# Optimization experiments

Measured on AMD Instinct MI355X. Metric: run time of the kernel, lower is better.

The kernel has to match this reference:

```python
import jax, jax.numpy as jnp
import numpy as np

N = 100000   # nodes
E = 3200000  # directed edges (avg degree 32)
T = 2048     # total flattened orders across all moves
M = 256      # number of moves (segments)


def _gat(x, src, dst, Wl, bl, Wr, br, att, b):
    # GATv2Conv (heads=1, eval mode -> attention dropout off), with self loops
    xl = x @ Wl.T + bl              # [N,10]
    xr = x @ Wr.T + br              # [N,10]
    sl = jnp.arange(N)
    s = jnp.concatenate([src, sl])
    d = jnp.concatenate([dst, sl])
    e = jax.nn.leaky_relu(xl[s] + xr[d], 0.2) @ att    # [E+N]
    emax = jax.ops.segment_max(e, d, num_segments=N)
    ex = jnp.exp(e - emax[d])
    den = jax.ops.segment_sum(ex, d, num_segments=N)
    return jax.ops.segment_sum((ex / den[d])[:, None] * xl[s], d, num_segments=N) + b


def setup_inputs() -> dict:
    key = jax.random.key(0)
    ks = iter(jax.random.split(key, 64))
    rn = lambda shape, s=0.1: jax.random.normal(next(ks), shape, jnp.float32) * s
    inp = {}
    inp['x1'] = rn((N, 15), 1.0)
    inp['x2'] = rn((1, 4), 1.0)
    src = jax.random.randint(next(ks), (E,), 0, N, jnp.int32)
    off = jax.random.randint(next(ks), (E,), 1, N, jnp.int32)
    inp['edge_src'] = src
    inp['edge_dst'] = ((src + off) % N).astype(jnp.int32)
    inp['move_type'] = jax.random.randint(next(ks), (T,), 0, 2, jnp.int32)
    inp['m_src'] = jax.random.randint(next(ks), (T,), 0, N, jnp.int32)
    inp['m_dst'] = jax.random.randint(next(ks), (T,), 0, N, jnp.int32)
    inp['m_target'] = jax.random.randint(next(ks), (T,), 0, N, jnp.int32)
    inp['m_armies'] = jax.random.uniform(next(ks), (T,), jnp.float32) * 10.0
    inp['move_id'] = (jnp.arange(T, dtype=jnp.int32) // (T // M))  # sorted, all segments non-empty
    # GATv2 layer params (in dims 15, 25, 25 -> out 10)
    for i, din in [(1, 15), (2, 25), (3, 25)]:
        inp[f'Wl{i}'] = rn((10, din)); inp[f'bl{i}'] = rn((10,))
        inp[f'Wr{i}'] = rn((10, din)); inp[f'br{i}'] = rn((10,))
        inp[f'att{i}'] = rn((10,));   inp[f'bias{i}'] = rn((10,))
    inp['lin_W'] = rn((15, 29)); inp['lin_b'] = rn((15,))
    inp['lin2_W'] = rn((1, 15)); inp['lin2_b'] = rn((1,))
    inp['aaa_W'] = rn((20, 48)); inp['aaa_b'] = rn((20,))
    inp['ccc_W'] = rn((20, 23)); inp['ccc_b'] = rn((20,))
    inp['attl_W'] = rn((1, 20)); inp['attl_b'] = rn((1,))
    inp['pi_W'] = rn((1, 20));   inp['pi_b'] = rn((1,))
    return inp


def reference(x1, x2, edge_src, edge_dst, move_type, m_src, m_dst, m_target, m_armies, move_id,
              Wl1, bl1, Wr1, br1, att1, bias1,
              Wl2, bl2, Wr2, br2, att2, bias2,
              Wl3, bl3, Wr3, br3, att3, bias3,
              lin_W, lin_b, lin2_W, lin2_b, aaa_W, aaa_b, ccc_W, ccc_b,
              attl_W, attl_b, pi_W, pi_b):
    h = jax.nn.relu(_gat(x1, edge_src, edge_dst, Wl1, bl1, Wr1, br1, att1, bias1))
    h = jax.nn.relu(_gat(jnp.concatenate([h, x1], 1), edge_src, edge_dst, Wl2, bl2, Wr2, br2, att2, bias2))
    x = jax.nn.relu(_gat(jnp.concatenate([h, x1], 1), edge_src, edge_dst, Wl3, bl3, Wr3, br3, att3, bias3))

    # per-order features (both branches computed, selected by move_type)
    extra = (0.6 * m_armies - 0.7 * (x1[m_dst, 3] + x1[m_dst, 4]))[:, None]
    feat_a = jnp.concatenate([x[m_src], x[m_dst], x1[m_src, 3:], x1[m_dst, 1:], m_armies[:, None], extra], axis=1)  # [T,48]
    a_out = jax.nn.relu(feat_a @ aaa_W.T + aaa_b)
    feat_d = jnp.concatenate([x[m_target], x1[m_target, 3:], m_armies[:, None]], axis=1)  # [T,23]
    d_out = jax.nn.relu(feat_d @ ccc_W.T + ccc_b)
    hm = jnp.where((move_type == 0)[:, None], a_out, d_out)  # [T,20]

    al = (hm @ attl_W.T + attl_b)[:, 0]   # [T]
    pi = (hm @ pi_W.T + pi_b)[:, 0]       # [T]
    amax = jax.ops.segment_max(al, move_id, num_segments=M)
    ex = jnp.exp(al - amax[move_id])
    den = jax.ops.segment_sum(ex, move_id, num_segments=M)
    p = jax.ops.segment_sum(ex / den[move_id] * pi, move_id, num_segments=M)  # [M]
    logp = jax.nn.log_softmax(p)

    x2t = jnp.tile(x2, (N, 1))
    v = jax.nn.relu(jnp.concatenate([x, x1, x2t], 1) @ lin_W.T + lin_b)
    V = jnp.tanh(jnp.mean(v @ lin2_W.T + lin2_b))
    return (V, logp)
```

## Files before the change

kernel.cpp:

```cpp
#include <hip/hip_runtime.h>
#include <cmath>

#define NN 100000
#define NE 3200000
#define TT 2048
#define MM 256
#define STR 16
#define HSTR 16
#define BSZ 64
#define NB 1563
#define EPB 16384
#define NBLK 196
#define SCAP 3072

__device__ __forceinline__ void atomicMaxF(float* addr, float v) {
    if (v >= 0.f) atomicMax((int*)addr, __float_as_int(v));
    else          atomicMin((unsigned int*)addr, __float_as_uint(v));
}

__device__ __forceinline__ unsigned short f2bf(float x) {
    unsigned u = __float_as_uint(x);
    u += 0x7FFFu + ((u >> 16) & 1u);
    return (unsigned short)(u >> 16);
}

__device__ __forceinline__ void unpack10(uint4 q, unsigned q2, float* a) {
    a[0] = __uint_as_float(q.x << 16);
    a[1] = __uint_as_float(q.x & 0xFFFF0000u);
    a[2] = __uint_as_float(q.y << 16);
    a[3] = __uint_as_float(q.y & 0xFFFF0000u);
    a[4] = __uint_as_float(q.z << 16);
    a[5] = __uint_as_float(q.z & 0xFFFF0000u);
    a[6] = __uint_as_float(q.w << 16);
    a[7] = __uint_as_float(q.w & 0xFFFF0000u);
    a[8] = __uint_as_float(q2 << 16);
    a[9] = __uint_as_float(q2 & 0xFFFF0000u);
}

__global__ __launch_bounds__(1024) void init_kernel(int* bcounts, float* amax, float* den_m,
                                                    float* num_m, float* Vsum) {
    int i = blockIdx.x * 1024 + threadIdx.x;
    if (i < NB) bcounts[i] = 0;
    if (i < MM) { amax[i] = -INFINITY; den_m[i] = 0.f; num_m[i] = 0.f; }
    if (i == 0) Vsum[0] = 0.f;
}

__global__ __launch_bounds__(256) void hist_kernel(const int* __restrict__ dst,
                                                   int* __restrict__ bcounts) {
    __shared__ int h[NB];
    int tid = threadIdx.x;
    for (int i = tid; i < NB; i += 256) h[i] = 0;
    __syncthreads();
    int base = blockIdx.x * EPB;
    int end = base + EPB; if (end > NE) end = NE;
    for (int i = base + tid * 4; i < end; i += 1024) {
        int4 d4 = *(const int4*)(dst + i);
        atomicAdd(&h[d4.x >> 6], 1);
        atomicAdd(&h[d4.y >> 6], 1);
        atomicAdd(&h[d4.z >> 6], 1);
        atomicAdd(&h[d4.w >> 6], 1);
    }
    __syncthreads();
    for (int i = tid; i < NB; i += 256) { int n = h[i]; if (n) atomicAdd(&bcounts[i], n); }
}

__global__ __launch_bounds__(1024) void scan_kernel(const int* __restrict__ bcounts,
                                                    int* __restrict__ bstart,
                                                    int* __restrict__ bcursor) {
    __shared__ int ssum[1024];
    int tid = threadIdx.x;
    const int per = (NB + 1023) / 1024;
    int base = tid * per;
    int s = 0;
    for (int i = 0; i < per; i++) {
        int idx = base + i;
        if (idx < NB) s += bcounts[idx];
    }
    ssum[tid] = s;
    __syncthreads();
    for (int off = 1; off < 1024; off <<= 1) {
        int v = (tid >= off) ? ssum[tid - off] : 0;
        __syncthreads();
        ssum[tid] += v;
        __syncthreads();
    }
    int run = ssum[tid] - s;
    for (int i = 0; i < per; i++) {
        int idx = base + i;
        if (idx < NB) {
            bstart[idx] = run;
            bcursor[idx] = run;
            run += bcounts[idx];
        }
    }
    if (tid == 0) bstart[NB] = NE;
}

__global__ __launch_bounds__(256) void scatter_kernel(const int* __restrict__ src,
                                                      const int* __restrict__ dst,
                                                      int* __restrict__ bcursor,
                                                      int* __restrict__ srt) {
    __shared__ int h[NB];
    __shared__ int c[NB];
    int tid = threadIdx.x;
    for (int i = tid; i < NB; i += 256) h[i] = 0;
    __syncthreads();
    int base = blockIdx.x * EPB;
    int end = base + EPB; if (end > NE) end = NE;
    for (int i = base + tid * 4; i < end; i += 1024) {
        int4 d4 = *(const int4*)(dst + i);
        atomicAdd(&h[d4.x >> 6], 1);
        atomicAdd(&h[d4.y >> 6], 1);
        atomicAdd(&h[d4.z >> 6], 1);
        atomicAdd(&h[d4.w >> 6], 1);
    }
    __syncthreads();
    for (int i = tid; i < NB; i += 256) {
        int n = h[i];
        h[i] = n ? atomicAdd(&bcursor[i], n) : 0;
        c[i] = 0;
    }
    __syncthreads();
    for (int i = base + tid * 4; i < end; i += 1024) {
        int4 d4 = *(const int4*)(dst + i);
        int4 s4 = *(const int4*)(src + i);
        int d, b, off;
        d = d4.x; b = d >> 6; off = atomicAdd(&c[b], 1); srt[h[b] + off] = ((d & 63) << 17) | s4.x;
        d = d4.y; b = d >> 6; off = atomicAdd(&c[b], 1); srt[h[b] + off] = ((d & 63) << 17) | s4.y;
        d = d4.z; b = d >> 6; off = atomicAdd(&c[b], 1); srt[h[b] + off] = ((d & 63) << 17) | s4.z;
        d = d4.w; b = d >> 6; off = atomicAdd(&c[b], 1); srt[h[b] + off] = ((d & 63) << 17) | s4.w;
    }
}

__global__ __launch_bounds__(256) void sort2_kernel(int* __restrict__ srt,
                                                    const int* __restrict__ bstart) {
    __shared__ int ent[SCAP];
    __shared__ int ent2[SCAP];
    __shared__ int cnts[BSZ];
    __shared__ int curs[BSZ];
    int b = blockIdx.x, tid = threadIdx.x;
    int i0 = bstart[b], i1 = bstart[b + 1];
    int cnt = i1 - i0;
    if (cnt > SCAP) cnt = SCAP;
    if (tid < BSZ) cnts[tid] = 0;
    __syncthreads();
    for (int i = tid; i < cnt; i += 256) {
        int p = srt[i0 + i];
        ent[i] = p;
        atomicAdd(&cnts[p >> 17], 1);
    }
    __syncthreads();
    if (tid == 0) {
        int run = 0;
        for (int k = 0; k < BSZ; k++) { curs[k] = run; run += cnts[k]; }
    }
    __syncthreads();
    for (int i = tid; i < cnt; i += 256) {
        int p = ent[i];
        int pos = atomicAdd(&curs[p >> 17], 1);
        ent2[pos] = p;
    }
    __syncthreads();
    for (int i = tid; i < cnt; i += 256) srt[i0 + i] = ent2[i];
}

__global__ __launch_bounds__(256) void prep_kernel(
    const float* __restrict__ hprev,
    const float* __restrict__ x1,
    const float* __restrict__ Wl, const float* __restrict__ bl,
    const float* __restrict__ Wr, const float* __restrict__ br,
    unsigned short* __restrict__ xlh,
    unsigned short* __restrict__ xrh,
    int din)
{
    __shared__ float sWl[250], sWr[250], sbl[10], sbr[10];
    int tid = threadIdx.x;
    int nw = 10 * din;
    for (int i = tid; i < nw; i += blockDim.x) { sWl[i] = Wl[i]; sWr[i] = Wr[i]; }
    if (tid < 10) { sbl[tid] = bl[tid]; sbr[tid] = br[tid]; }
    __syncthreads();
    int n = blockIdx.x * blockDim.x + tid;
    if (n >= NN) return;

    float in[25];
    if (din == 15) {
        #pragma unroll
        for (int k = 0; k < 15; k++) in[k] = x1[n * 15 + k];
    } else {
        #pragma unroll
        for (int k = 0; k < 10; k++) in[k] = hprev[n * STR + k];
        #pragma unroll
        for (int k = 0; k < 15; k++) in[10 + k] = x1[n * 15 + k];
    }

    float slv[10], srv[10];
    #pragma unroll
    for (int j = 0; j < 10; j++) {
        float sl = sbl[j], sr = sbr[j];
        for (int k = 0; k < din; k++) {
            sl += in[k] * sWl[j * din + k];
            sr += in[k] * sWr[j * din + k];
        }
        slv[j] = sl; srv[j] = sr;
    }
    unsigned* lp = (unsigned*)(xlh + n * HSTR);
    unsigned* rp = (unsigned*)(xrh + n * HSTR);
    #pragma unroll
    for (int j = 0; j < 5; j++) {
        lp[j] = (unsigned)f2bf(slv[2 * j]) | ((unsigned)f2bf(slv[2 * j + 1]) << 16);
        rp[j] = (unsigned)f2bf(srv[2 * j]) | ((unsigned)f2bf(srv[2 * j + 1]) << 16);
    }
}

__global__ __launch_bounds__(256, 4) void gather_kernel(
    const int* __restrict__ srt, const int* __restrict__ bstart,
    const unsigned short* __restrict__ xlh, const unsigned short* __restrict__ xrh,
    const float* __restrict__ att, const float* __restrict__ bias,
    float* __restrict__ hout)
{
    __shared__ float accs[BSZ * 11];
    __shared__ float xrs[BSZ * 11];
    __shared__ float sat[10];
    int b = blockIdx.x, tid = threadIdx.x;
    if (tid < 10) sat[tid] = att[tid];
    __syncthreads();

    int n0 = b * BSZ;
    if (tid < BSZ) {
        int n = n0 + tid;
        if (n < NN) {
            const unsigned short* lr = xlh + n * HSTR;
            const unsigned short* rr = xrh + n * HSTR;
            uint4 ql = *(const uint4*)lr;  unsigned ql2 = *(const unsigned*)(lr + 8);
            uint4 qr = *(const uint4*)rr;  unsigned qr2 = *(const unsigned*)(rr + 8);
            float a[10], r[10];
            unpack10(ql, ql2, a);
            unpack10(qr, qr2, r);
            #pragma unroll
            for (int k = 0; k < 10; k++) xrs[tid * 11 + k] = r[k];
            float e = 0.f;
            #pragma unroll
            for (int k = 0; k < 10; k++) {
                float t = a[k] + r[k];
                t = t > 0.f ? t : 0.2f * t;
                e += sat[k] * t;
            }
            float ex = __expf(e);
            #pragma unroll
            for (int k = 0; k < 10; k++) accs[tid * 11 + k] = ex * a[k];
            accs[tid * 11 + 10] = ex;
        } else {
            #pragma unroll
            for (int k = 0; k < 11; k++) { accs[tid * 11 + k] = 0.f; xrs[tid * 11 + k] = 0.f; }
        }
    }
    __syncthreads();

    int i0 = bstart[b], i1 = bstart[b + 1];
    int cnt = i1 - i0;
    int C = (cnt + 255) >> 8;
    int a0 = i0 + tid * C;
    int a1 = a0 + C; if (a1 > i1) a1 = i1;
    if (a0 < a1) {
        int p = srt[a0];
        const unsigned short* row0 = xlh + (p & 0x1FFFF) * HSTR;
        uint4 q = *(const uint4*)row0;
        unsigned q2 = *(const unsigned*)(row0 + 8);
        int cur = p >> 17;
        float racc[10];
        #pragma unroll
        for (int k = 0; k < 10; k++) racc[k] = 0.f;
        float rden = 0.f;
        for (int i = a0; i < a1; i++) {
            int pn = p; uint4 qn = q; unsigned q2n = q2;
            if (i + 1 < a1) {
                pn = srt[i + 1];
                const unsigned short* rn = xlh + (pn & 0x1FFFF) * HSTR;
                qn = *(const uint4*)rn;
                q2n = *(const unsigned*)(rn + 8);
            }
            int ld = p >> 17;
            if (ld != cur) {
                float* ac = accs + cur * 11;
                #pragma unroll
                for (int k = 0; k < 10; k++) atomicAdd(ac + k, racc[k]);
                atomicAdd(ac + 10, rden);
                #pragma unroll
                for (int k = 0; k < 10; k++) racc[k] = 0.f;
                rden = 0.f;
                cur = ld;
            }
            float a[10];
            unpack10(q, q2, a);
            const float* r = xrs + ld * 11;
            float e = 0.f;
            #pragma unroll
            for (int k = 0; k < 10; k++) {
                float t = a[k] + r[k];
                t = t > 0.f ? t : 0.2f * t;
                e += sat[k] * t;
            }
            float ex = __expf(e);
            rden += ex;
            #pragma unroll
            for (int k = 0; k < 10; k++) racc[k] += ex * a[k];
            p = pn; q = qn; q2 = q2n;
        }
        float* ac = accs + cur * 11;
        #pragma unroll
        for (int k = 0; k < 10; k++) atomicAdd(ac + k, racc[k]);
        atomicAdd(ac + 10, rden);
    }
    __syncthreads();

    if (tid < BSZ) {
        int n = n0 + tid;
        if (n < NN) {
            float inv = 1.f / accs[tid * 11 + 10];
            #pragma unroll
            for (int k = 0; k < 10; k++) {
                float v = accs[tid * 11 + k] * inv + bias[k];
                hout[n * STR + k] = v > 0.f ? v : 0.f;
            }
        }
    }
}

__global__ __launch_bounds__(256) void value_kernel(
    const float* __restrict__ x, const float* __restrict__ x1, const float* __restrict__ x2,
    const float* __restrict__ lin_W, const float* __restrict__ lin_b,
    const float* __restrict__ lin2_W, const float* __restrict__ lin2_b,
    float* __restrict__ Vsum)
{
    __shared__ float sW[15 * 29], sb[15], sW2[15];
    __shared__ float red[256];
    int tid = threadIdx.x;
    for (int i = tid; i < 15 * 29; i += 256) sW[i] = lin_W[i];
    if (tid < 15) { sb[tid] = lin_b[tid]; sW2[tid] = lin2_W[tid]; }
    __syncthreads();
    int n = blockIdx.x * 256 + tid;
    float local = 0.f;
    if (n < NN) {
        float in[29];
        #pragma unroll
        for (int k = 0; k < 10; k++) in[k] = x[n * STR + k];
        #pragma unroll
        for (int k = 0; k < 15; k++) in[10 + k] = x1[n * 15 + k];
        #pragma unroll
        for (int k = 0; k < 4; k++) in[25 + k] = x2[k];
        float sc = lin2_b[0];
        #pragma unroll
        for (int j = 0; j < 15; j++) {
            float s = sb[j];
            for (int k = 0; k < 29; k++) s += in[k] * sW[j * 29 + k];
            sc += (s > 0.f ? s : 0.f) * sW2[j];
        }
        local = sc;
    }
    red[tid] = local;
    __syncthreads();
    for (int off = 128; off > 0; off >>= 1) {
        if (tid < off) red[tid] += red[tid + off];
        __syncthreads();
    }
    if (tid == 0) atomicAdd(Vsum, red[0]);
}

__global__ __launch_bounds__(256) void orders_kernel(
    const float* __restrict__ x, const float* __restrict__ x1,
    const int* __restrict__ move_type, const int* __restrict__ m_src,
    const int* __restrict__ m_dst, const int* __restrict__ m_target,
    const float* __restrict__ m_armies, const int* __restrict__ move_id,
    const float* __restrict__ aaa_W, const float* __restrict__ aaa_b,
    const float* __restrict__ ccc_W, const float* __restrict__ ccc_b,
    const float* __restrict__ attl_W, const float* __restrict__ attl_b,
    const float* __restrict__ pi_W, const float* __restrict__ pi_b,
    float* __restrict__ al_out, float* __restrict__ pi_out, float* __restrict__ amax)
{
    __shared__ float sA[20 * 48], sC[20 * 23], sAb[20], sCb[20];
    int tid = threadIdx.x;
    for (int i = tid; i < 20 * 48; i += 256) sA[i] = aaa_W[i];
    for (int i = tid; i < 20 * 23; i += 256) sC[i] = ccc_W[i];
    if (tid < 20) { sAb[tid] = aaa_b[tid]; sCb[tid] = ccc_b[tid]; }
    __syncthreads();
    int t = blockIdx.x * 256 + tid;
    if (t >= TT) return;

    float armies = m_armies[t];
    float hm[20];
    if (move_type[t] == 0) {
        int sn = m_src[t], dn = m_dst[t];
        float f[48];
        #pragma unroll
        for (int k = 0; k < 10; k++) f[k] = x[sn * STR + k];
        #pragma unroll
        for (int k = 0; k < 10; k++) f[10 + k] = x[dn * STR + k];
        #pragma unroll
        for (int k = 0; k < 12; k++) f[20 + k] = x1[sn * 15 + 3 + k];
        #pragma unroll
        for (int k = 0; k < 14; k++) f[32 + k] = x1[dn * 15 + 1 + k];
        f[46] = armies;
        f[47] = 0.6f * armies - 0.7f * (x1[dn * 15 + 3] + x1[dn * 15 + 4]);
        #pragma unroll
        for (int j = 0; j < 20; j++) {
            float s = sAb[j];
            for (int k = 0; k < 48; k++) s += f[k] * sA[j * 48 + k];
            hm[j] = s > 0.f ? s : 0.f;
        }
    } else {
        int tg = m_target[t];
        float f[23];
        #pragma unroll
        for (int k = 0; k < 10; k++) f[k] = x[tg * STR + k];
        #pragma unroll
        for (int k = 0; k < 12; k++) f[10 + k] = x1[tg * 15 + 3 + k];
        f[22] = armies;
        #pragma unroll
        for (int j = 0; j < 20; j++) {
            float s = sCb[j];
            for (int k = 0; k < 23; k++) s += f[k] * sC[j * 23 + k];
            hm[j] = s > 0.f ? s : 0.f;
        }
    }
    float a = attl_b[0], p = pi_b[0];
    #pragma unroll
    for (int j = 0; j < 20; j++) { a += hm[j] * attl_W[j]; p += hm[j] * pi_W[j]; }
    al_out[t] = a;
    pi_out[t] = p;
    atomicMaxF(&amax[move_id[t]], a);
}

__global__ __launch_bounds__(256) void orders2_kernel(
    const float* __restrict__ al, const float* __restrict__ piv,
    const int* __restrict__ move_id, const float* __restrict__ amax,
    float* __restrict__ den_m, float* __restrict__ num_m)
{
    int t = blockIdx.x * 256 + threadIdx.x;
    if (t >= TT) return;
    int m = move_id[t];
    float ex = __expf(al[t] - amax[m]);
    atomicAdd(den_m + m, ex);
    atomicAdd(num_m + m, ex * piv[t]);
}

__global__ __launch_bounds__(256) void final_kernel(
    const float* __restrict__ num_m, const float* __restrict__ den_m,
    const float* __restrict__ Vsum, float* __restrict__ out)
{
    __shared__ float sh[256];
    __shared__ float s_max, s_sum;
    int m = threadIdx.x;
    float p = num_m[m] / den_m[m];
    sh[m] = p;
    __syncthreads();
    for (int off = 128; off > 0; off >>= 1) {
        if (m < off) sh[m] = fmaxf(sh[m], sh[m + off]);
        __syncthreads();
    }
    if (m == 0) s_max = sh[0];
    __syncthreads();
    float e = __expf(p - s_max);
    sh[m] = e;
    __syncthreads();
    for (int off = 128; off > 0; off >>= 1) {
        if (m < off) sh[m] += sh[m + off];
        __syncthreads();
    }
    if (m == 0) s_sum = sh[0];
    __syncthreads();
    out[1 + m] = p - s_max - logf(s_sum);
    if (m == 0) out[0] = tanhf(Vsum[0] / (float)NN);
}

extern "C" void kernel_launch(void* const* d_in, const int* in_sizes, int n_in,
                              void* d_out, int out_size, void* d_ws, size_t ws_size,
                              hipStream_t stream) {
    const float* x1        = (const float*)d_in[0];
    const float* x2        = (const float*)d_in[1];
    const int*   esrc      = (const int*)d_in[2];
    const int*   edst      = (const int*)d_in[3];
    const int*   move_type = (const int*)d_in[4];
    const int*   m_src     = (const int*)d_in[5];
    const int*   m_dst     = (const int*)d_in[6];
    const int*   m_target  = (const int*)d_in[7];
    const float* m_armies  = (const float*)d_in[8];
    const int*   move_id   = (const int*)d_in[9];
    const float* W[3][6];
    for (int l = 0; l < 3; l++)
        for (int j = 0; j < 6; j++)
            W[l][j] = (const float*)d_in[10 + l * 6 + j];
    const float* lin_W  = (const float*)d_in[28];
    const float* lin_b  = (const float*)d_in[29];
    const float* lin2_W = (const float*)d_in[30];
    const float* lin2_b = (const float*)d_in[31];
    const float* aaa_W  = (const float*)d_in[32];
    const float* aaa_b  = (const float*)d_in[33];
    const float* ccc_W  = (const float*)d_in[34];
    const float* ccc_b  = (const float*)d_in[35];
    const float* attl_W = (const float*)d_in[36];
    const float* attl_b = (const float*)d_in[37];
    const float* pi_W   = (const float*)d_in[38];
    const float* pi_b   = (const float*)d_in[39];

    float* ws = (float*)d_ws;
    float* hA    = ws; ws += NN * STR;
    float* al    = ws; ws += TT;
    float* piv   = ws; ws += TT;
    float* amax  = ws; ws += MM;
    float* den_m = ws; ws += MM;
    float* num_m = ws; ws += MM;
    float* Vsum  = ws; ws += 1;
    unsigned short* xlh = (unsigned short*)ws; ws += NN * HSTR / 2;
    unsigned short* xrh = (unsigned short*)ws; ws += NN * HSTR / 2;
    int* iws = (int*)ws;
    int* bcounts = iws; iws += NB;
    int* bstart  = iws; iws += NB + 1;
    int* bcursor = iws; iws += NB;
    int* srt     = iws; iws += NE;

    dim3 blk(256);
    dim3 gN((NN + 255) / 256);
    dim3 gT(TT / 256);

    init_kernel<<<dim3(2), dim3(1024), 0, stream>>>(bcounts, amax, den_m, num_m, Vsum);
    hist_kernel<<<dim3(NBLK), blk, 0, stream>>>(edst, bcounts);
    scan_kernel<<<dim3(1), dim3(1024), 0, stream>>>(bcounts, bstart, bcursor);
    scatter_kernel<<<dim3(NBLK), blk, 0, stream>>>(esrc, edst, bcursor, srt);
    sort2_kernel<<<dim3(NB), blk, 0, stream>>>(srt, bstart);

    prep_kernel<<<gN, blk, 0, stream>>>(nullptr, x1, W[0][0], W[0][1], W[0][2], W[0][3], xlh, xrh, 15);
    gather_kernel<<<dim3(NB), blk, 0, stream>>>(srt, bstart, xlh, xrh, W[0][4], W[0][5], hA);

    prep_kernel<<<gN, blk, 0, stream>>>(hA, x1, W[1][0], W[1][1], W[1][2], W[1][3], xlh, xrh, 25);
    gather_kernel<<<dim3(NB), blk, 0, stream>>>(srt, bstart, xlh, xrh, W[1][4], W[1][5], hA);

    prep_kernel<<<gN, blk, 0, stream>>>(hA, x1, W[2][0], W[2][1], W[2][2], W[2][3], xlh, xrh, 25);
    gather_kernel<<<dim3(NB), blk, 0, stream>>>(srt, bstart, xlh, xrh, W[2][4], W[2][5], hA);

    value_kernel<<<gN, blk, 0, stream>>>(hA, x1, x2, lin_W, lin_b, lin2_W, lin2_b, Vsum);
    orders_kernel<<<gT, blk, 0, stream>>>(hA, x1, move_type, m_src, m_dst, m_target,
                                          m_armies, move_id, aaa_W, aaa_b, ccc_W, ccc_b,
                                          attl_W, attl_b, pi_W, pi_b, al, piv, amax);
    orders2_kernel<<<gT, blk, 0, stream>>>(al, piv, move_id, amax, den_m, num_m);
    final_kernel<<<dim3(1), blk, 0, stream>>>(num_m, den_m, Vsum, (float*)d_out);
}
```

Measured before the change: 476.2 us.

## Pad per-block scatter chunks to 16 and unroll gather with preloaded indices

```diff
diff --git a/kernel.cpp b/kernel.cpp
--- a/kernel.cpp
+++ b/kernel.cpp
@@ -12,6 +12,9 @@
 #define EPB 16384
 #define NBLK 196
 #define SCAP 3072
+#define PCAP 4096
+#define CMAX 12
+#define SRTP_CAP 5500000
 
 __device__ __forceinline__ void atomicMaxF(float* addr, float v) {
     if (v >= 0.f) atomicMax((int*)addr, __float_as_int(v));
@@ -37,16 +40,17 @@
     a[9] = __uint_as_float(q2 & 0xFFFF0000u);
 }
 
-__global__ __launch_bounds__(1024) void init_kernel(int* bcounts, float* amax, float* den_m,
-                                                    float* num_m, float* Vsum) {
+__global__ __launch_bounds__(1024) void init_kernel(int* bcounts, int* pcounts, float* amax,
+                                                    float* den_m, float* num_m, float* Vsum) {
     int i = blockIdx.x * 1024 + threadIdx.x;
-    if (i < NB) bcounts[i] = 0;
+    if (i < NB) { bcounts[i] = 0; pcounts[i] = 0; }
     if (i < MM) { amax[i] = -INFINITY; den_m[i] = 0.f; num_m[i] = 0.f; }
     if (i == 0) Vsum[0] = 0.f;
 }
 
 __global__ __launch_bounds__(256) void hist_kernel(const int* __restrict__ dst,
-                                                   int* __restrict__ bcounts) {
+                                                   int* __restrict__ bcounts,
+                                                   int* __restrict__ pcounts) {
     __shared__ int h[NB];
     int tid = threadIdx.x;
     for (int i = tid; i < NB; i += 256) h[i] = 0;
@@ -61,45 +65,56 @@
         atomicAdd(&h[d4.w >> 6], 1);
     }
     __syncthreads();
-    for (int i = tid; i < NB; i += 256) { int n = h[i]; if (n) atomicAdd(&bcounts[i], n); }
+    for (int i = tid; i < NB; i += 256) {
+        int n = h[i];
+        if (n) {
+            atomicAdd(&bcounts[i], n);
+            atomicAdd(&pcounts[i], (n + 15) & ~15);
+        }
+    }
 }
 
 __global__ __launch_bounds__(1024) void scan_kernel(const int* __restrict__ bcounts,
+                                                    const int* __restrict__ pcounts,
                                                     int* __restrict__ bstart,
-                                                    int* __restrict__ bcursor) {
+                                                    int* __restrict__ pbstart,
+                                                    int* __restrict__ pcursor) {
     __shared__ int ssum[1024];
+    __shared__ int psum[1024];
     int tid = threadIdx.x;
     const int per = (NB + 1023) / 1024;
     int base = tid * per;
-    int s = 0;
+    int s = 0, p = 0;
     for (int i = 0; i < per; i++) {
         int idx = base + i;
-        if (idx < NB) s += bcounts[idx];
-    }
-    ssum[tid] = s;
+        if (idx < NB) { s += bcounts[idx]; p += pcounts[idx]; }
+    }
+    ssum[tid] = s; psum[tid] = p;
     __syncthreads();
     for (int off = 1; off < 1024; off <<= 1) {
         int v = (tid >= off) ? ssum[tid - off] : 0;
+        int w = (tid >= off) ? psum[tid - off] : 0;
         __syncthreads();
-        ssum[tid] += v;
+        ssum[tid] += v; psum[tid] += w;
         __syncthreads();
     }
     int run = ssum[tid] - s;
+    int prun = psum[tid] - p;
     for (int i = 0; i < per; i++) {
         int idx = base + i;
         if (idx < NB) {
-            bstart[idx] = run;
-            bcursor[idx] = run;
-            run += bcounts[idx];
-        }
-    }
-    if (tid == 0) bstart[NB] = NE;
+            bstart[idx] = run;              run += bcounts[idx];
+            pbstart[idx] = prun;
+            pcursor[idx] = prun;            prun += pcounts[idx];
+        }
+    }
+    if (tid == 0) { bstart[NB] = NE; pbstart[NB] = psum[1023]; }
 }
 
 __global__ __launch_bounds__(256) void scatter_kernel(const int* __restrict__ src,
                                                       const int* __restrict__ dst,
-                                                      int* __restrict__ bcursor,
-                                                      int* __restrict__ srt) {
+                                                      int* __restrict__ pcursor,
+                                                      int* __restrict__ srtp) {
     __shared__ int h[NB];
     __shared__ int c[NB];
     int tid = threadIdx.x;
@@ -117,7 +132,7 @@
     __syncthreads();
     for (int i = tid; i < NB; i += 256) {
         int n = h[i];
-        h[i] = n ? atomicAdd(&bcursor[i], n) : 0;
+        h[i] = n ? atomicAdd(&pcursor[i], (n + 15) & ~15) : 0;
         c[i] = 0;
     }
     __syncthreads();
@@ -125,29 +140,40 @@
         int4 d4 = *(const int4*)(dst + i);
         int4 s4 = *(const int4*)(src + i);
         int d, b, off;
-        d = d4.x; b = d >> 6; off = atomicAdd(&c[b], 1); srt[h[b] + off] = ((d & 63) << 17) | s4.x;
-        d = d4.y; b = d >> 6; off = atomicAdd(&c[b], 1); srt[h[b] + off] = ((d & 63) << 17) | s4.y;
-        d = d4.z; b = d >> 6; off = atomicAdd(&c[b], 1); srt[h[b] + off] = ((d & 63) << 17) | s4.z;
-        d = d4.w; b = d >> 6; off = atomicAdd(&c[b], 1); srt[h[b] + off] = ((d & 63) << 17) | s4.w;
-    }
-}
-
-__global__ __launch_bounds__(256) void sort2_kernel(int* __restrict__ srt,
-                                                    const int* __restrict__ bstart) {
-    __shared__ int ent[SCAP];
+        d = d4.x; b = d >> 6; off = atomicAdd(&c[b], 1); srtp[h[b] + off] = ((d & 63) << 17) | s4.x;
+        d = d4.y; b = d >> 6; off = atomicAdd(&c[b], 1); srtp[h[b] + off] = ((d & 63) << 17) | s4.y;
+        d = d4.z; b = d >> 6; off = atomicAdd(&c[b], 1); srtp[h[b] + off] = ((d & 63) << 17) | s4.z;
+        d = d4.w; b = d >> 6; off = atomicAdd(&c[b], 1); srtp[h[b] + off] = ((d & 63) << 17) | s4.w;
+    }
+    __syncthreads();
+    for (int i = tid; i < NB; i += 256) {
+        int n = c[i];
+        if (n) {
+            int pad = (16 - (n & 15)) & 15;
+            int baseo = h[i] + n;
+            for (int k = 0; k < pad; k++) srtp[baseo + k] = -1;
+        }
+    }
+}
+
+__global__ __launch_bounds__(256) void sort2_kernel(const int* __restrict__ srtp,
+                                                    const int* __restrict__ pbstart,
+                                                    const int* __restrict__ bstart,
+                                                    int* __restrict__ srt) {
+    __shared__ int ent[PCAP];
     __shared__ int ent2[SCAP];
     __shared__ int cnts[BSZ];
     __shared__ int curs[BSZ];
     int b = blockIdx.x, tid = threadIdx.x;
-    int i0 = bstart[b], i1 = bstart[b + 1];
-    int cnt = i1 - i0;
-    if (cnt > SCAP) cnt = SCAP;
+    int p0 = pbstart[b], p1 = pbstart[b + 1];
+    int pcnt = p1 - p0;
+    if (pcnt > PCAP) pcnt = PCAP;
     if (tid < BSZ) cnts[tid] = 0;
     __syncthreads();
-    for (int i = tid; i < cnt; i += 256) {
-        int p = srt[i0 + i];
+    for (int i = tid; i < pcnt; i += 256) {
+        int p = srtp[p0 + i];
         ent[i] = p;
-        atomicAdd(&cnts[p >> 17], 1);
+        if (p >= 0) atomicAdd(&cnts[p >> 17], 1);
     }
     __syncthreads();
     if (tid == 0) {
@@ -155,12 +181,16 @@
         for (int k = 0; k < BSZ; k++) { curs[k] = run; run += cnts[k]; }
     }
     __syncthreads();
-    for (int i = tid; i < cnt; i += 256) {
+    for (int i = tid; i < pcnt; i += 256) {
         int p = ent[i];
-        int pos = atomicAdd(&curs[p >> 17], 1);
-        ent2[pos] = p;
-    }
-    __syncthreads();
+        if (p >= 0) {
+            int pos = atomicAdd(&curs[p >> 17], 1);
+            ent2[pos] = p;
+        }
+    }
+    __syncthreads();
+    int i0 = bstart[b];
+    int cnt = bstart[b + 1] - i0;
     for (int i = tid; i < cnt; i += 256) srt[i0 + i] = ent2[i];
 }
 
@@ -261,25 +291,30 @@
     int C = (cnt + 255) >> 8;
     int a0 = i0 + tid * C;
     int a1 = a0 + C; if (a1 > i1) a1 = i1;
-    if (a0 < a1) {
-        int p = srt[a0];
-        const unsigned short* row0 = xlh + (p & 0x1FFFF) * HSTR;
+    int len = a1 - a0; if (len < 0) len = 0;
+    if (len > 0) {
+        int ps[CMAX];
+        #pragma unroll
+        for (int i = 0; i < CMAX; i++) ps[i] = (i < len) ? srt[a0 + i] : -1;
+
+        const unsigned short* row0 = xlh + (ps[0] & 0x1FFFF) * HSTR;
         uint4 q = *(const uint4*)row0;
         unsigned q2 = *(const unsigned*)(row0 + 8);
-        int cur = p >> 17;
+        int cur = ps[0] >> 17;
         float racc[10];
         #pragma unroll
         for (int k = 0; k < 10; k++) racc[k] = 0.f;
         float rden = 0.f;
-        for (int i = a0; i < a1; i++) {
-            int pn = p; uint4 qn = q; unsigned q2n = q2;
-            if (i + 1 < a1) {
-                pn = srt[i + 1];
-                const unsigned short* rn = xlh + (pn & 0x1FFFF) * HSTR;
+        #pragma unroll
+        for (int i = 0; i < CMAX; i++) {
+            if (i >= len) break;
+            uint4 qn = q; unsigned q2n = q2;
+            if (i + 1 < len) {
+                const unsigned short* rn = xlh + (ps[i + 1] & 0x1FFFF) * HSTR;
                 qn = *(const uint4*)rn;
                 q2n = *(const unsigned*)(rn + 8);
             }
-            int ld = p >> 17;
+            int ld = ps[i] >> 17;
             if (ld != cur) {
                 float* ac = accs + cur * 11;
                 #pragma unroll
@@ -304,7 +339,7 @@
             rden += ex;
             #pragma unroll
             for (int k = 0; k < 10; k++) racc[k] += ex * a[k];
-            p = pn; q = qn; q2 = q2n;
+            q = qn; q2 = q2n;
         }
         float* ac = accs + cur * 11;
         #pragma unroll
@@ -514,19 +549,22 @@
     unsigned short* xrh = (unsigned short*)ws; ws += NN * HSTR / 2;
     int* iws = (int*)ws;
     int* bcounts = iws; iws += NB;
+    int* pcounts = iws; iws += NB;
     int* bstart  = iws; iws += NB + 1;
-    int* bcursor = iws; iws += NB;
+    int* pbstart = iws; iws += NB + 1;
+    int* pcursor = iws; iws += NB;
     int* srt     = iws; iws += NE;
+    int* srtp    = iws; iws += SRTP_CAP;
 
     dim3 blk(256);
     dim3 gN((NN + 255) / 256);
     dim3 gT(TT / 256);
 
-    init_kernel<<<dim3(2), dim3(1024), 0, stream>>>(bcounts, amax, den_m, num_m, Vsum);
-    hist_kernel<<<dim3(NBLK), blk, 0, stream>>>(edst, bcounts);
-    scan_kernel<<<dim3(1), dim3(1024), 0, stream>>>(bcounts, bstart, bcursor);
-    scatter_kernel<<<dim3(NBLK), blk, 0, stream>>>(esrc, edst, bcursor, srt);
-    sort2_kernel<<<dim3(NB), blk, 0, stream>>>(srt, bstart);
+    init_kernel<<<dim3(2), dim3(1024), 0, stream>>>(bcounts, pcounts, amax, den_m, num_m, Vsum);
+    hist_kernel<<<dim3(NBLK), blk, 0, stream>>>(edst, bcounts, pcounts);
+    scan_kernel<<<dim3(1), dim3(1024), 0, stream>>>(bcounts, pcounts, bstart, pbstart, pcursor);
+    scatter_kernel<<<dim3(NBLK), blk, 0, stream>>>(esrc, edst, pcursor, srtp);
+    sort2_kernel<<<dim3(NB), blk, 0, stream>>>(srtp, pbstart, bstart, srt);
 
     prep_kernel<<<gN, blk, 0, stream>>>(nullptr, x1, W[0][0], W[0][1], W[0][2], W[0][3], xlh, xrh, 15);
     gather_kernel<<<dim3(NB), blk, 0, stream>>>(srt, bstart, xlh, xrh, W[0][4], W[0][5], hA);
```

Measured after the change: 464.4 us. -2.5%, faster.
